# Optimization experiments

Measured on AMD Instinct MI355X. Metric: run time of the kernel, lower is better.

The kernel has to match this reference:

```python
import jax, jax.numpy as jnp
import numpy as np

B, S, DIM = 2, 2048, 2048
NH, NKV = 32, 8
HD = DIM // NH          # 64
NREP = NH // NKV        # 4
BASE = 10000.0


def setup_inputs() -> dict:
    key = jax.random.key(0)
    ks = jax.random.split(key, 5)
    x = jax.random.normal(ks[0], (B, S, DIM), dtype=jnp.float32)
    # causal mask, 1 = keep, 0 = masked (matches masked_fill(mask == 0, -inf))
    mask = jnp.tril(jnp.ones((S, S), dtype=jnp.float32))[None, None]
    scale = 0.02
    Wq = jax.random.normal(ks[1], (DIM, NH * HD), dtype=jnp.float32) * scale
    Wk = jax.random.normal(ks[2], (DIM, NKV * HD), dtype=jnp.float32) * scale
    Wv = jax.random.normal(ks[3], (DIM, NKV * HD), dtype=jnp.float32) * scale
    Wo = jax.random.normal(ks[4], (NH * HD, DIM), dtype=jnp.float32) * scale
    return {"x": x, "mask": mask, "Wq": Wq, "Wk": Wk, "Wv": Wv, "Wo": Wo}


def _rope_cos_sin(seq_len, head_dim, dtype):
    inv_freq = 1.0 / (BASE ** (jnp.arange(0, head_dim, 2, dtype=jnp.float32) / head_dim))
    t = jnp.arange(seq_len, dtype=jnp.float32)
    freqs = t[:, None] * inv_freq[None, :]            # [S, HD/2]
    return jnp.cos(freqs).astype(dtype), jnp.sin(freqs).astype(dtype)


def _apply_rope(x, cos, sin):
    # x: [B, H, S, HD]; cos/sin: [S, HD/2] broadcast over B,H
    x1, x2 = jnp.split(x, 2, axis=-1)
    c = cos[None, None]
    s = sin[None, None]
    return jnp.concatenate([x1 * c - x2 * s, x2 * c + x1 * s], axis=-1)


def reference(x, mask, Wq, Wk, Wv, Wo):
    b, s, _ = x.shape
    q = (x @ Wq).reshape(b, s, NH, HD).transpose(0, 2, 1, 3)   # [B,NH,S,HD]
    k = (x @ Wk).reshape(b, s, NKV, HD).transpose(0, 2, 1, 3)  # [B,NKV,S,HD]
    v = (x @ Wv).reshape(b, s, NKV, HD).transpose(0, 2, 1, 3)
    cos, sin = _rope_cos_sin(s, HD, x.dtype)
    q = _apply_rope(q, cos, sin)
    k = _apply_rope(k, cos, sin)
    # GQA: repeat kv heads
    k = jnp.repeat(k, NREP, axis=1)
    v = jnp.repeat(v, NREP, axis=1)
    scale = HD ** -0.5
    attn = jnp.einsum('bhqd,bhkd->bhqk', q, k) * scale
    attn = jnp.where(mask == 0, -jnp.inf, attn)
    attn = jax.nn.softmax(attn, axis=-1)
    out = jnp.einsum('bhqk,bhkd->bhqd', attn, v)
    out = out.transpose(0, 2, 1, 3).reshape(b, s, NH * HD)
    return out @ Wo
```

## Files before the change

### kernel.cpp

```cpp
#include <hip/hip_runtime.h>
#include <stdint.h>

typedef __attribute__((ext_vector_type(8))) short short8;
typedef __attribute__((ext_vector_type(4))) short short4v;
typedef __attribute__((ext_vector_type(4))) float float4v;
typedef __attribute__((ext_vector_type(16))) float f32x16;
typedef __attribute__((ext_vector_type(4))) int int4v;
typedef __attribute__((ext_vector_type(2))) int int2v;

#define DEV __device__ __forceinline__

DEV ushort f2bf(float f){
  uint32_t u = __float_as_uint(f);
  u = (u + 0x7fffu + ((u >> 16) & 1u)) >> 16;
  return (ushort)u;
}
DEV float bf2f(ushort h){
  uint32_t u = ((uint32_t)h) << 16;
  return __uint_as_float(u);
}

DEV void gload16(const void* g, void* l){
  __builtin_amdgcn_global_load_lds((const __attribute__((address_space(1))) void*)g,
                                   (__attribute__((address_space(3))) void*)l, 16, 0, 0);
}

DEV uint32_t cvtpk(float lo, float hi){
  uint32_t d;
  asm("v_cvt_pk_bf16_f32 %0, %1, %2" : "=v"(d) : "v"(lo), "v"(hi));
  return d;
}

__global__ __launch_bounds__(256) void k_prep(const float* __restrict__ x, const float* __restrict__ Wq,
                                              const float* __restrict__ Wk, const float* __restrict__ Wv,
                                              const float* __restrict__ Wo,
                                              ushort* __restrict__ xb, ushort* __restrict__ wqkvt,
                                              ushort* __restrict__ wot,
                                              float* __restrict__ cost, float* __restrict__ sint,
                                              float qscale){
  __shared__ float tile[32][33];
  const int bid = blockIdx.x;
  if (bid < 10240){
    const float* src; ushort* dst; int N, K, bx, by; float scale;
    if (bid < 4096){ src = Wq; dst = wqkvt; N = 2048; K = 2048; scale = qscale; bx = bid & 63; by = bid >> 6; }
    else if (bid < 5120){ int lb = bid - 4096; src = Wk; dst = wqkvt + (size_t)2048 * 2048; N = 512; K = 2048; scale = 1.f; bx = lb & 15; by = lb >> 4; }
    else if (bid < 6144){ int lb = bid - 5120; src = Wv; dst = wqkvt + (size_t)2560 * 2048; N = 512; K = 2048; scale = 1.f; bx = lb & 15; by = lb >> 4; }
    else { int lb = bid - 6144; src = Wo; dst = wot; N = 2048; K = 2048; scale = 1.f; bx = lb & 63; by = lb >> 6; }
    int c0 = bx * 32, r0 = by * 32;
    int tx = threadIdx.x & 31, ty = threadIdx.x >> 5;
    #pragma unroll
    for (int i = 0; i < 32; i += 8)
      tile[ty + i][tx] = src[(size_t)(r0 + ty + i) * N + (c0 + tx)];
    __syncthreads();
    #pragma unroll
    for (int i = 0; i < 32; i += 8)
      dst[(size_t)(c0 + ty + i) * K + (r0 + tx)] = f2bf(tile[tx][ty + i] * scale);
  } else if (bid < 10496){
    int i = (bid - 10240) * 256 + threadIdx.x;
    int s = i >> 5, d = i & 31;
    float inv = powf(10000.0f, -(float)d / 32.0f);
    float ang = (float)s * inv;
    float sv, cv;
    sincosf(ang, &sv, &cv);
    cost[i] = cv;
    sint[i] = sv;
  } else {
    int i = (bid - 10496) * 256 + threadIdx.x;
    float4v v = *(const float4v*)(x + (size_t)i * 4);
    short4v o;
    o[0] = (short)f2bf(v[0]); o[1] = (short)f2bf(v[1]);
    o[2] = (short)f2bf(v[2]); o[3] = (short)f2bf(v[3]);
    *(short4v*)(xb + (size_t)i * 4) = o;
  }
}

template<int BM, int BN, bool OUTF32>
__global__ __launch_bounds__(512, 2) void k_gemm8(const ushort* __restrict__ A, const ushort* __restrict__ Bt,
                                                  void* __restrict__ Cp, int M, int N, int K, int nbx){
  constexpr int WM = BM / 2, WN = BN / 4;
  constexpr int MR = WM / 16, NR = WN / 16, MP = MR / 4;
  constexpr int AISS = BM / 64, BISS = BN / 64, ISS = AISS + BISS;
  constexpr int BUFB = (BM + BN) * 128;
  __shared__ char lds[2 * BUFB];

  int wg = blockIdx.x;
  int cpx = (int)gridDim.x >> 3;
  wg = (wg & 7) * cpx + (wg >> 3);
  const int bn = wg % nbx, bm = wg / nbx;
  const int tid = threadIdx.x;
  const int w = tid >> 6, l = tid & 63, l15 = l & 15, hi = l >> 4;
  const int wr = w >> 2, wc = w & 3;

  const int r8 = tid >> 3;
  const int ce = ((tid & 7) ^ (r8 & 7)) << 3;
  const ushort* ag = A + (size_t)(bm * BM + r8) * K + ce;
  const ushort* bg = Bt + (size_t)(bn * BN + r8) * K + ce;

  float4v acc[MR][NR];
  #pragma unroll
  for (int a = 0; a < MR; ++a)
    #pragma unroll
    for (int b = 0; b < NR; ++b)
      acc[a][b] = (float4v){0.f, 0.f, 0.f, 0.f};

  auto stage = [&](int kt, int buf){
    char* ab = lds + buf * BUFB;
    char* bb = ab + BM * 128;
    #pragma unroll
    for (int i = 0; i < AISS; ++i)
      gload16(ag + (size_t)(i * 64) * K + kt * 64, ab + i * 8192 + tid * 16);
    #pragma unroll
    for (int i = 0; i < BISS; ++i)
      gload16(bg + (size_t)(i * 64) * K + kt * 64, bb + i * 8192 + tid * 16);
  };
  auto lda = [&](const char* ab, int mf, int kk)->short8{
    int row = wr * WM + mf * 16 + l15;
    int a = (row * 128 + kk * 64 + hi * 16) ^ ((row & 7) << 4);
    return *(const short8*)(ab + a);
  };
  auto ldb = [&](const char* bb, int nf, int kk)->short8{
    int row = wc * WN + nf * 16 + l15;
    int a = (row * 128 + kk * 64 + hi * 16) ^ ((row & 7) << 4);
    return *(const short8*)(bb + a);
  };

  const int nkt = K >> 6;
  stage(0, 0);
  for (int t = 0; t < nkt; ++t){
    if (t + 1 < nkt){
      stage(t + 1, (t + 1) & 1);
      if constexpr (ISS == 8)      asm volatile("s_waitcnt vmcnt(8)" ::: "memory");
      else if constexpr (ISS == 7) asm volatile("s_waitcnt vmcnt(7)" ::: "memory");
      else                         asm volatile("s_waitcnt vmcnt(6)" ::: "memory");
    } else {
      asm volatile("s_waitcnt vmcnt(0)" ::: "memory");
    }
    __builtin_amdgcn_s_barrier();
    __builtin_amdgcn_sched_barrier(0);

    const char* ab = lds + (t & 1) * BUFB;
    const char* bb = ab + BM * 128;
    short8 bfr[NR][2];
    #pragma unroll
    for (int nf = 0; nf < NR; ++nf){ bfr[nf][0] = ldb(bb, nf, 0); bfr[nf][1] = ldb(bb, nf, 1); }
    short8 af[MP][2];
    #pragma unroll
    for (int ml = 0; ml < MP; ++ml){ af[ml][0] = lda(ab, ml, 0); af[ml][1] = lda(ab, ml, 1); }

    #pragma unroll
    for (int p = 0; p < 4; ++p){
      __builtin_amdgcn_s_barrier();
      asm volatile("s_waitcnt lgkmcnt(0)" ::: "memory");
      __builtin_amdgcn_sched_barrier(0);
      __builtin_amdgcn_s_setprio(1);
      #pragma unroll
      for (int ml = 0; ml < MP; ++ml)
        #pragma unroll
        for (int nf = 0; nf < NR; ++nf){
          const int mf = p * MP + ml;
          acc[mf][nf] = __builtin_amdgcn_mfma_f32_16x16x32_bf16(af[ml][0], bfr[nf][0], acc[mf][nf], 0, 0, 0);
          acc[mf][nf] = __builtin_amdgcn_mfma_f32_16x16x32_bf16(af[ml][1], bfr[nf][1], acc[mf][nf], 0, 0, 0);
        }
      __builtin_amdgcn_s_setprio(0);
      __builtin_amdgcn_sched_barrier(0);
      if (p < 3){
        #pragma unroll
        for (int ml = 0; ml < MP; ++ml){
          af[ml][0] = lda(ab, (p + 1) * MP + ml, 0);
          af[ml][1] = lda(ab, (p + 1) * MP + ml, 1);
        }
      }
      __builtin_amdgcn_s_barrier();
    }
  }

  #pragma unroll
  for (int mf = 0; mf < MR; ++mf){
    int row0 = bm * BM + wr * WM + mf * 16 + hi * 4;
    #pragma unroll
    for (int nf = 0; nf < NR; ++nf){
      int col = bn * BN + wc * WN + nf * 16 + l15;
      #pragma unroll
      for (int reg = 0; reg < 4; ++reg){
        size_t idx = (size_t)(row0 + reg) * N + col;
        if constexpr (OUTF32) ((float*)Cp)[idx] = acc[mf][nf][reg];
        else                  ((ushort*)Cp)[idx] = f2bf(acc[mf][nf][reg]);
      }
    }
  }
}

__global__ __launch_bounds__(256) void k_rope_vt(ushort* __restrict__ qkv, const float* __restrict__ cost,
                                                 const float* __restrict__ sint, ushort* __restrict__ vt){
  __shared__ ushort tile[64][72];
  const int bid = blockIdx.x;
  if (bid < 5120){
    int t = bid * 256 + threadIdx.x;
    int row = t / 320;
    int rem = t - row * 320;
    int head = rem >> 3, d0 = (rem & 7) * 4;
    int s = row & 2047;
    ushort* p = qkv + (size_t)row * 3072 + head * 64 + d0;
    short4v a = *(short4v*)p;
    short4v b = *(short4v*)(p + 32);
    float4v c  = *(const float4v*)(cost + s * 32 + d0);
    float4v sn = *(const float4v*)(sint + s * 32 + d0);
    short4v na, nb;
    #pragma unroll
    for (int j = 0; j < 4; ++j){
      float x1 = bf2f((ushort)a[j]), x2 = bf2f((ushort)b[j]);
      na[j] = (short)f2bf(x1 * c[j] - x2 * sn[j]);
      nb[j] = (short)f2bf(x2 * c[j] + x1 * sn[j]);
    }
    *(short4v*)p = na;
    *(short4v*)(p + 32) = nb;
  } else {
    int lb = bid - 5120;
    int g = lb >> 5, st = lb & 31;
    int b = g >> 3, hk = g & 7;
    const ushort* src = qkv + (size_t)(b * 2048 + st * 64) * 3072 + 2560 + hk * 64;
    int tid = threadIdx.x;
    #pragma unroll
    for (int i = 0; i < 2; ++i){
      int r = i * 32 + (tid >> 3), c8 = (tid & 7) * 8;
      short8 v = *(const short8*)(src + (size_t)r * 3072 + c8);
      #pragma unroll
      for (int j = 0; j < 8; ++j) tile[r][c8 + j] = (ushort)v[j];
    }
    __syncthreads();
    ushort* dst = vt + (size_t)g * 64 * 2048 + st * 64;
    #pragma unroll
    for (int i = 0; i < 2; ++i){
      int d = i * 32 + (tid >> 3), s8 = (tid & 7) * 8;
      short8 ov;
      #pragma unroll
      for (int j = 0; j < 8; ++j) ov[j] = (short)tile[s8 + j][d];
      *(short8*)(dst + (size_t)d * 2048 + s8) = ov;
    }
  }
}

__global__ __launch_bounds__(256) void k_attn3(const ushort* __restrict__ qkv, const ushort* __restrict__ vt,
                                               ushort* __restrict__ att){
  __shared__ ushort K_lds[2][64 * 64];
  __shared__ ushort V_lds[2][64 * 64];
  const int raw = blockIdx.x;
  const int xcd = raw & 7, slot = raw >> 3;
  const int qb = 15 - (slot >> 3);
  const int rem = slot & 7;
  const int gidx = xcd * 2 + (rem >> 2);
  const int b = gidx >> 3, hk = gidx & 7;
  const int h = hk * 4 + (rem & 3);
  const int tid = threadIdx.x;
  const int w = tid >> 6, l = tid & 63, ql = l & 31, g = l >> 5;
  const int qw = qb * 128 + w * 32;
  const int diag_t = (qw + 31) >> 6;
  const int swz = (ql & 7) << 4;

  short8 qf[4];
  {
    const ushort* qbase = qkv + (size_t)(b * 2048 + qw + ql) * 3072 + h * 64 + g * 8;
    #pragma unroll
    for (int ds = 0; ds < 4; ++ds) qf[ds] = *(const short8*)(qbase + ds * 16);
  }

  f32x16 o0, o1;
  #pragma unroll
  for (int r = 0; r < 16; ++r){ o0[r] = 0.f; o1[r] = 0.f; }
  float m_run = -3e38f, l_part = 0.f;

  const ushort* kbase = qkv + (size_t)(b * 2048) * 3072 + 2048 + hk * 64;
  const ushort* vbase = vt + (size_t)gidx * 64 * 2048;
  const int nt = qb * 2 + 2;
  const int srow = tid >> 3, scol = (tid & 7) * 8;
  const int swrsw = (srow & 7) << 4;

  #pragma unroll
  for (int i = 0; i < 2; ++i){
    int r = i * 32 + srow;
    short8 kv = *(const short8*)(kbase + (size_t)r * 3072 + scol);
    short8 vv = *(const short8*)(vbase + (size_t)r * 2048 + scol);
    *(short8*)((char*)K_lds[0] + r * 128 + ((scol * 2) ^ swrsw)) = kv;
    *(short8*)((char*)V_lds[0] + r * 128 + ((scol * 2) ^ swrsw)) = vv;
  }
  __syncthreads();

  int cur = 0;
  for (int t = 0; t < nt; ++t){
    short8 kpre[2], vpre[2];
    const bool more = (t + 1 < nt);
    if (more){
      const ushort* kb = kbase + (size_t)(t + 1) * 64 * 3072;
      const ushort* vb = vbase + (t + 1) * 64;
      #pragma unroll
      for (int i = 0; i < 2; ++i){
        int r = i * 32 + srow;
        kpre[i] = *(const short8*)(kb + (size_t)r * 3072 + scol);
        vpre[i] = *(const short8*)(vb + (size_t)r * 2048 + scol);
      }
    }

    if (t <= diag_t){
      f32x16 sa0, sa1;
      #pragma unroll
      for (int r = 0; r < 16; ++r){ sa0[r] = 0.f; sa1[r] = 0.f; }
      __builtin_amdgcn_s_setprio(1);
      #pragma unroll
      for (int ds = 0; ds < 4; ++ds){
        int cb = (ds * 32 + g * 16) ^ swz;
        short8 k0 = *(const short8*)((const char*)K_lds[cur] + ql * 128 + cb);
        short8 k1 = *(const short8*)((const char*)K_lds[cur] + (32 + ql) * 128 + cb);
        sa0 = __builtin_amdgcn_mfma_f32_32x32x16_bf16(k0, qf[ds], sa0, 0, 0, 0);
        sa1 = __builtin_amdgcn_mfma_f32_32x32x16_bf16(k1, qf[ds], sa1, 0, 0, 0);
      }
      __builtin_amdgcn_s_setprio(0);

      if (t == diag_t){
        int thr = qw + ql - t * 64;
        #pragma unroll
        for (int r = 0; r < 16; ++r){
          int kl = (r & 3) + 8 * (r >> 2) + 4 * g;
          sa0[r] = (kl > thr) ? -3e38f : sa0[r];
          sa1[r] = (kl + 32 > thr) ? -3e38f : sa1[r];
        }
      }

      float mt = fmaxf(sa0[0], sa1[0]);
      #pragma unroll
      for (int r = 1; r < 16; ++r) mt = fmaxf(mt, fmaxf(sa0[r], sa1[r]));
      mt = fmaxf(mt, __shfl_xor(mt, 32, 64));

      if (__any(mt > m_run + 8.0f)){
        float mn = fmaxf(m_run, mt);
        float corr = __builtin_amdgcn_exp2f(m_run - mn);
        #pragma unroll
        for (int r = 0; r < 16; ++r){ o0[r] *= corr; o1[r] *= corr; }
        l_part *= corr;
        m_run = mn;
      }

      uint32_t wds[2][8];
      float ps0 = 0.f, ps1 = 0.f, ps2 = 0.f, ps3 = 0.f;
      #pragma unroll
      for (int r = 0; r < 16; ++r){
        float p0 = __builtin_amdgcn_exp2f(sa0[r] - m_run);
        float p1 = __builtin_amdgcn_exp2f(sa1[r] - m_run);
        sa0[r] = p0; sa1[r] = p1;
        if ((r & 1) == 0){ ps0 += p0; ps1 += p1; }
        else { ps2 += p0; ps3 += p1; }
      }
      l_part += (ps0 + ps2) + (ps1 + ps3);
      #pragma unroll
      for (int u = 0; u < 8; ++u){
        wds[0][u] = cvtpk(sa0[2 * u], sa0[2 * u + 1]);
        wds[1][u] = cvtpk(sa1[2 * u], sa1[2 * u + 1]);
      }

      __builtin_amdgcn_s_setprio(1);
      #pragma unroll
      for (int ks = 0; ks < 4; ++ks){
        const int s2 = ks >> 1, c4 = (ks & 1) * 4;
        uint32_t a0 = wds[s2][c4 + 0], a1 = wds[s2][c4 + 1];
        uint32_t b0 = wds[s2][c4 + 2], b1 = wds[s2][c4 + 3];
        uint32_t s0 = g ? a0 : b0, s1 = g ? a1 : b1;
        uint32_t r0 = (uint32_t)__shfl_xor((int)s0, 32, 64);
        uint32_t r1 = (uint32_t)__shfl_xor((int)s1, 32, 64);
        union { int4v w4; short8 s8; } pb;
        pb.w4[0] = g ? (int)r0 : (int)a0;
        pb.w4[1] = g ? (int)r1 : (int)a1;
        pb.w4[2] = g ? (int)b0 : (int)r0;
        pb.w4[3] = g ? (int)b1 : (int)r1;
        int cb = (ks * 32 + g * 16) ^ swz;
        short8 v0 = *(const short8*)((const char*)V_lds[cur] + ql * 128 + cb);
        short8 v1 = *(const short8*)((const char*)V_lds[cur] + (32 + ql) * 128 + cb);
        o0 = __builtin_amdgcn_mfma_f32_32x32x16_bf16(v0, pb.s8, o0, 0, 0, 0);
        o1 = __builtin_amdgcn_mfma_f32_32x32x16_bf16(v1, pb.s8, o1, 0, 0, 0);
      }
      __builtin_amdgcn_s_setprio(0);
    }

    if (more){
      int nxt = cur ^ 1;
      #pragma unroll
      for (int i = 0; i < 2; ++i){
        int r = i * 32 + srow;
        *(short8*)((char*)K_lds[nxt] + r * 128 + ((scol * 2) ^ swrsw)) = kpre[i];
        *(short8*)((char*)V_lds[nxt] + r * 128 + ((scol * 2) ^ swrsw)) = vpre[i];
      }
      __syncthreads();
      cur = nxt;
    }
  }

  float lf = l_part + __shfl_xor(l_part, 32, 64);
  float invl = 1.0f / lf;
  ushort* ob = att + (size_t)(b * 2048 + qw + ql) * 2048 + h * 64;
  #pragma unroll
  for (int dm = 0; dm < 2; ++dm){
    #pragma unroll
    for (int rg = 0; rg < 4; ++rg){
      float f0 = (dm ? o1[4 * rg + 0] : o0[4 * rg + 0]) * invl;
      float f1 = (dm ? o1[4 * rg + 1] : o0[4 * rg + 1]) * invl;
      float f2 = (dm ? o1[4 * rg + 2] : o0[4 * rg + 2]) * invl;
      float f3 = (dm ? o1[4 * rg + 3] : o0[4 * rg + 3]) * invl;
      int2v wv;
      wv[0] = (int)cvtpk(f0, f1);
      wv[1] = (int)cvtpk(f2, f3);
      int d0 = dm * 32 + 8 * rg + 4 * g;
      *(int2v*)(ob + d0) = wv;
    }
  }
}

extern "C" void kernel_launch(void* const* d_in, const int* in_sizes, int n_in,
                              void* d_out, int out_size, void* d_ws, size_t ws_size,
                              hipStream_t stream) {
  const float* x  = (const float*)d_in[0];
  const float* Wq = (const float*)d_in[2];
  const float* Wk = (const float*)d_in[3];
  const float* Wv = (const float*)d_in[4];
  const float* Wo = (const float*)d_in[5];

  char* ws = (char*)d_ws;
  ushort* xb    = (ushort*)(ws);
  ushort* wqkvt = (ushort*)(ws + (16u << 20));
  ushort* wot   = (ushort*)(ws + (28u << 20));
  ushort* qkv   = (ushort*)(ws + (36u << 20));
  ushort* att   = (ushort*)(ws + (60u << 20));
  ushort* vt    = (ushort*)(ws + (76u << 20));
  float*  cost  = (float*)(ws + (80u << 20));
  float*  sint  = (float*)(ws + (80u << 20) + 262144);

  const float qscale = 0.125f * 1.4426950408889634f;

  k_prep<<<18688, 256, 0, stream>>>(x, Wq, Wk, Wv, Wo, xb, wqkvt, wot, cost, sint, qscale);
  k_gemm8<256, 192, false><<<256, 512, 0, stream>>>(xb, wqkvt, qkv, 4096, 3072, 2048, 16);
  k_rope_vt<<<5632, 256, 0, stream>>>(qkv, cost, sint, vt);
  k_attn3<<<1024, 256, 0, stream>>>(qkv, vt, att);
  k_gemm8<128, 256, true><<<256, 512, 0, stream>>>(att, wot, d_out, 4096, 2048, 2048, 8);
}
```

Measured before the change: 187.9 us.

## Stream K/V tiles to LDS via direct global_load_lds and use permlane32 swaps

The attention kernel now stages K and V tiles straight from global memory into LDS with global_load_lds. The write-side swizzle moves into the global source address, which removes the register round trip and the explicit LDS stores. The loop syncs once per tile, waiting on vmcnt and a barrier, and then issues the next tile's async load into the other buffer. Cross-half reductions and the P-matrix exchange use permlane32_swap in place of shfl_xor plus selects, and the max reduction becomes a tree. This saves VGPRs and VALU/LDS traffic. The risk is that vmcnt(0) at the top of each iteration serialises the wait on the prefetch.

Result: no change. 185.8 us (-1.1%).

```diff
diff --git a/kernel.cpp b/kernel.cpp
--- a/kernel.cpp
+++ b/kernel.cpp
@@ -7,6 +7,7 @@
 typedef __attribute__((ext_vector_type(16))) float f32x16;
 typedef __attribute__((ext_vector_type(4))) int int4v;
 typedef __attribute__((ext_vector_type(2))) int int2v;
+typedef __attribute__((ext_vector_type(2))) unsigned int uint2v;
 
 #define DEV __device__ __forceinline__
 
@@ -29,6 +30,10 @@
   uint32_t d;
   asm("v_cvt_pk_bf16_f32 %0, %1, %2" : "=v"(d) : "v"(lo), "v"(hi));
   return d;
+}
+
+DEV uint2v plswap2(uint32_t a, uint32_t b){
+  return __builtin_amdgcn_permlane32_swap(a, b, false, false);
 }
 
 __global__ __launch_bounds__(256) void k_prep(const float* __restrict__ x, const float* __restrict__ Wq,
@@ -240,10 +245,9 @@
   }
 }
 
-__global__ __launch_bounds__(256) void k_attn3(const ushort* __restrict__ qkv, const ushort* __restrict__ vt,
+__global__ __launch_bounds__(256) void k_attn6(const ushort* __restrict__ qkv, const ushort* __restrict__ vt,
                                                ushort* __restrict__ att){
-  __shared__ ushort K_lds[2][64 * 64];
-  __shared__ ushort V_lds[2][64 * 64];
+  __shared__ __align__(16) char lds[2][16384];
   const int raw = blockIdx.x;
   const int xcd = raw & 7, slot = raw >> 3;
   const int qb = 15 - (slot >> 3);
@@ -269,38 +273,33 @@
   for (int r = 0; r < 16; ++r){ o0[r] = 0.f; o1[r] = 0.f; }
   float m_run = -3e38f, l_part = 0.f;
 
-  const ushort* kbase = qkv + (size_t)(b * 2048) * 3072 + 2048 + hk * 64;
-  const ushort* vbase = vt + (size_t)gidx * 64 * 2048;
+  const int srow = tid >> 3;
+  const int ce = ((tid & 7) ^ (srow & 7)) << 3;
+  const ushort* kg = qkv + (size_t)(b * 2048 + srow) * 3072 + 2048 + hk * 64 + ce;
+  const ushort* vg = vt + (size_t)gidx * 64 * 2048 + (size_t)srow * 2048 + ce;
   const int nt = qb * 2 + 2;
-  const int srow = tid >> 3, scol = (tid & 7) * 8;
-  const int swrsw = (srow & 7) << 4;
-
-  #pragma unroll
-  for (int i = 0; i < 2; ++i){
-    int r = i * 32 + srow;
-    short8 kv = *(const short8*)(kbase + (size_t)r * 3072 + scol);
-    short8 vv = *(const short8*)(vbase + (size_t)r * 2048 + scol);
-    *(short8*)((char*)K_lds[0] + r * 128 + ((scol * 2) ^ swrsw)) = kv;
-    *(short8*)((char*)V_lds[0] + r * 128 + ((scol * 2) ^ swrsw)) = vv;
-  }
-  __syncthreads();
-
-  int cur = 0;
+
+  auto stage = [&](int t, int buf){
+    char* lb = lds[buf];
+    #pragma unroll
+    for (int i = 0; i < 2; ++i)
+      gload16(kg + (size_t)(t * 64 + i * 32) * 3072, lb + i * 4096 + tid * 16);
+    #pragma unroll
+    for (int i = 0; i < 2; ++i)
+      gload16(vg + (size_t)(i * 32) * 2048 + t * 64, lb + 8192 + i * 4096 + tid * 16);
+  };
+
+  stage(0, 0);
   for (int t = 0; t < nt; ++t){
-    short8 kpre[2], vpre[2];
-    const bool more = (t + 1 < nt);
-    if (more){
-      const ushort* kb = kbase + (size_t)(t + 1) * 64 * 3072;
-      const ushort* vb = vbase + (t + 1) * 64;
-      #pragma unroll
-      for (int i = 0; i < 2; ++i){
-        int r = i * 32 + srow;
-        kpre[i] = *(const short8*)(kb + (size_t)r * 3072 + scol);
-        vpre[i] = *(const short8*)(vb + (size_t)r * 2048 + scol);
-      }
-    }
+    asm volatile("s_waitcnt vmcnt(0)" ::: "memory");
+    __builtin_amdgcn_s_barrier();
+    __builtin_amdgcn_sched_barrier(0);
+    if (t + 1 < nt) stage(t + 1, (t + 1) & 1);
 
     if (t <= diag_t){
+      const char* Kb = lds[t & 1];
+      const char* Vb = Kb + 8192;
+
       f32x16 sa0, sa1;
       #pragma unroll
       for (int r = 0; r < 16; ++r){ sa0[r] = 0.f; sa1[r] = 0.f; }
@@ -308,8 +307,8 @@
       #pragma unroll
       for (int ds = 0; ds < 4; ++ds){
         int cb = (ds * 32 + g * 16) ^ swz;
-        short8 k0 = *(const short8*)((const char*)K_lds[cur] + ql * 128 + cb);
-        short8 k1 = *(const short8*)((const char*)K_lds[cur] + (32 + ql) * 128 + cb);
+        short8 k0 = *(const short8*)(Kb + ql * 128 + cb);
+        short8 k1 = *(const short8*)(Kb + (32 + ql) * 128 + cb);
         sa0 = __builtin_amdgcn_mfma_f32_32x32x16_bf16(k0, qf[ds], sa0, 0, 0, 0);
         sa1 = __builtin_amdgcn_mfma_f32_32x32x16_bf16(k1, qf[ds], sa1, 0, 0, 0);
       }
@@ -325,10 +324,18 @@
         }
       }
 
-      float mt = fmaxf(sa0[0], sa1[0]);
-      #pragma unroll
-      for (int r = 1; r < 16; ++r) mt = fmaxf(mt, fmaxf(sa0[r], sa1[r]));
-      mt = fmaxf(mt, __shfl_xor(mt, 32, 64));
+      float mx[16];
+      #pragma unroll
+      for (int r = 0; r < 16; ++r) mx[r] = fmaxf(sa0[r], sa1[r]);
+      #pragma unroll
+      for (int s = 8; s > 0; s >>= 1)
+        #pragma unroll
+        for (int r = 0; r < s; ++r) mx[r] = fmaxf(mx[r], mx[r + s]);
+      float mt = mx[0];
+      {
+        uint2v mm = plswap2(__float_as_uint(mt), __float_as_uint(mt));
+        mt = fmaxf(__uint_as_float(mm[0]), __uint_as_float(mm[1]));
+      }
 
       if (__any(mt > m_run + 8.0f)){
         float mn = fmaxf(m_run, mt);
@@ -360,39 +367,26 @@
       #pragma unroll
       for (int ks = 0; ks < 4; ++ks){
         const int s2 = ks >> 1, c4 = (ks & 1) * 4;
-        uint32_t a0 = wds[s2][c4 + 0], a1 = wds[s2][c4 + 1];
-        uint32_t b0 = wds[s2][c4 + 2], b1 = wds[s2][c4 + 3];
-        uint32_t s0 = g ? a0 : b0, s1 = g ? a1 : b1;
-        uint32_t r0 = (uint32_t)__shfl_xor((int)s0, 32, 64);
-        uint32_t r1 = (uint32_t)__shfl_xor((int)s1, 32, 64);
+        uint2v e0 = plswap2(wds[s2][c4 + 0], wds[s2][c4 + 2]);
+        uint2v e1 = plswap2(wds[s2][c4 + 1], wds[s2][c4 + 3]);
         union { int4v w4; short8 s8; } pb;
-        pb.w4[0] = g ? (int)r0 : (int)a0;
-        pb.w4[1] = g ? (int)r1 : (int)a1;
-        pb.w4[2] = g ? (int)b0 : (int)r0;
-        pb.w4[3] = g ? (int)b1 : (int)r1;
+        pb.w4[0] = (int)e0[0]; pb.w4[1] = (int)e1[0];
+        pb.w4[2] = (int)e0[1]; pb.w4[3] = (int)e1[1];
         int cb = (ks * 32 + g * 16) ^ swz;
-        short8 v0 = *(const short8*)((const char*)V_lds[cur] + ql * 128 + cb);
-        short8 v1 = *(const short8*)((const char*)V_lds[cur] + (32 + ql) * 128 + cb);
+        short8 v0 = *(const short8*)(Vb + ql * 128 + cb);
+        short8 v1 = *(const short8*)(Vb + (32 + ql) * 128 + cb);
         o0 = __builtin_amdgcn_mfma_f32_32x32x16_bf16(v0, pb.s8, o0, 0, 0, 0);
         o1 = __builtin_amdgcn_mfma_f32_32x32x16_bf16(v1, pb.s8, o1, 0, 0, 0);
       }
       __builtin_amdgcn_s_setprio(0);
     }
-
-    if (more){
-      int nxt = cur ^ 1;
-      #pragma unroll
-      for (int i = 0; i < 2; ++i){
-        int r = i * 32 + srow;
-        *(short8*)((char*)K_lds[nxt] + r * 128 + ((scol * 2) ^ swrsw)) = kpre[i];
-        *(short8*)((char*)V_lds[nxt] + r * 128 + ((scol * 2) ^ swrsw)) = vpre[i];
-      }
-      __syncthreads();
-      cur = nxt;
-    }
-  }
-
-  float lf = l_part + __shfl_xor(l_part, 32, 64);
+  }
+
+  float lf;
+  {
+    uint2v lm = plswap2(__float_as_uint(l_part), __float_as_uint(l_part));
+    lf = __uint_as_float(lm[0]) + __uint_as_float(lm[1]);
+  }
   float invl = 1.0f / lf;
   ushort* ob = att + (size_t)(b * 2048 + qw + ql) * 2048 + h * 64;
   #pragma unroll
@@ -436,6 +430,6 @@
   k_prep<<<18688, 256, 0, stream>>>(x, Wq, Wk, Wv, Wo, xb, wqkvt, wot, cost, sint, qscale);
   k_gemm8<256, 192, false><<<256, 512, 0, stream>>>(xb, wqkvt, qkv, 4096, 3072, 2048, 16);
   k_rope_vt<<<5632, 256, 0, stream>>>(qkv, cost, sint, vt);
-  k_attn3<<<1024, 256, 0, stream>>>(qkv, vt, att);
+  k_attn6<<<1024, 256, 0, stream>>>(qkv, vt, att);
   k_gemm8<128, 256, true><<<256, 512, 0, stream>>>(att, wot, d_out, 4096, 2048, 2048, 8);
 }
```
